# Kernel optimization log

Hardware: AMD Instinct MI355X
Metric: run time of the kernel (lower is better)

## Reference

```python
import jax, jax.numpy as jnp
import numpy as np

N, E, D_IN, H, D = 170000, 1200000, 128, 4, 32
NEG_SLOPE = 0.2


def setup_inputs() -> dict:
    key = jax.random.key(0)
    ks = jax.random.split(key, 8)
    x = jax.random.normal(ks[0], (N, D_IN), dtype=jnp.float32)
    # xavier-normal-ish scale for linear weights
    W_embed = jax.random.normal(ks[1], (D_IN, H * D), dtype=jnp.float32) * (2.0 / (D_IN + H * D)) ** 0.5
    a_src = jax.random.normal(ks[2], (H, D), dtype=jnp.float32) * (2.0 / (1 + H * D)) ** 0.5
    a_dst = jax.random.normal(ks[3], (H, D), dtype=jnp.float32) * (2.0 / (1 + H * D)) ** 0.5
    W_lin = jax.random.normal(ks[4], (D_IN, H * D), dtype=jnp.float32) * (2.0 / (D_IN + H * D)) ** 0.5
    bias = jnp.zeros((H * D,), dtype=jnp.float32)
    src = jax.random.randint(ks[5], (E,), 0, N, dtype=jnp.int32)
    dst = jax.random.randint(ks[6], (E,), 0, N, dtype=jnp.int32)
    return {"x": x, "W_embed": W_embed, "a_src": a_src, "a_dst": a_dst,
            "W_lin": W_lin, "bias": bias, "src": src, "dst": dst}


def reference(x, W_embed, a_src, a_dst, W_lin, bias, src, dst):
    n = x.shape[0]
    # node projections: [N, H, D]
    h = (x @ W_embed).reshape(n, H, D)
    dot_src = jnp.einsum('nhd,hd->nh', h, a_src)  # [N, H]
    dot_dst = jnp.einsum('nhd,hd->nh', h, a_dst)  # [N, H]
    # edge attention logits: leaky_relu(dot_src[u] + dot_dst[v])  [E, H]
    z = dot_src[src] + dot_dst[dst]
    logit = jnp.where(z >= 0, z, NEG_SLOPE * z)
    # edge softmax over incoming edges of each destination node
    m = jax.ops.segment_max(logit, dst, num_segments=n)          # [N, H]
    e = jnp.exp(logit - m[dst])                                   # [E, H]
    denom = jax.ops.segment_sum(e, dst, num_segments=n)          # [N, H]
    prob = e / denom[dst]                                         # [E, H]
    # weighted scatter-sum aggregation: sum_e prob_e * h[src_e]
    msg = h[src] * prob[:, :, None]                               # [E, H, D]
    out = jax.ops.segment_sum(msg, dst, num_segments=n)          # [N, H, D]
    out = out.reshape(n, H * D)
    out = out + x @ W_lin
    out = out + bias[None, :]
    return out
```

## Files before the change

### kernel.cpp

```cpp
#include <hip/hip_runtime.h>
#include <hip/hip_bf16.h>

static constexpr int   N_NODES   = 170000;
static constexpr int   E_EDGES   = 1200000;
static constexpr float NEG_SLOPE = 0.2f;

typedef __attribute__((ext_vector_type(8))) short bfrag8;
typedef __attribute__((ext_vector_type(4))) float facc4;

__device__ __forceinline__ short f2bf(float f) {
    __hip_bfloat16 h = __float2bfloat16(f);
    return *reinterpret_cast<short*>(&h);
}

__global__ void wt_init_kernel(const float* __restrict__ We,
                               const float* __restrict__ Wl,
                               const float* __restrict__ a_src,
                               const float* __restrict__ a_dst,
                               short* __restrict__ WtG,
                               int* __restrict__ deg)
{
    const int t = threadIdx.x;
    if (blockIdx.x < 128) {
        const int k = blockIdx.x;
        if (t < 128) WtG[t * 128 + k] = f2bf(We[k * 128 + t]);
        else         WtG[t * 128 + k] = f2bf(Wl[k * 128 + (t - 128)]);
    } else if (blockIdx.x < 136) {
        const int idx = (blockIdx.x - 128) * 256 + t;
        if (idx < 1024) {
            const int g = idx >> 7;
            const int k = idx & 127;
            const int hh = g & 3;
            const float* av = (g < 4) ? a_src : a_dst;
            float s = 0.f;
            #pragma unroll
            for (int d = 0; d < 32; ++d)
                s += We[k * 128 + hh * 32 + d] * av[hh * 32 + d];
            WtG[(256 + g) * 128 + k] = f2bf(s);
        } else {
            const int z = idx - 1024;
            WtG[(264 + (z >> 7)) * 128 + (z & 127)] = 0;
        }
    }
    const int i = blockIdx.x * 256 + t;
    if (i < N_NODES) deg[i] = 0;
}

__global__ void hist_kernel(const int* __restrict__ dst,
                            int* __restrict__ deg,
                            int* __restrict__ seq)
{
    int e = blockIdx.x * blockDim.x + threadIdx.x;
    if (e < E_EDGES) {
        const int s = atomicAdd(&deg[dst[e]], 1);
        __builtin_nontemporal_store(s, &seq[e]);
    }
}

__global__ __launch_bounds__(256) void scan_local_kernel(
    const int* __restrict__ deg, int* __restrict__ row_ptr, int* __restrict__ bsum)
{
    __shared__ int sh[256];
    const int t = threadIdx.x;
    const int base = blockIdx.x * 1024 + t * 4;
    int v0 = (base + 0 < N_NODES) ? deg[base + 0] : 0;
    int v1 = (base + 1 < N_NODES) ? deg[base + 1] : 0;
    int v2 = (base + 2 < N_NODES) ? deg[base + 2] : 0;
    int v3 = (base + 3 < N_NODES) ? deg[base + 3] : 0;
    const int tot = v0 + v1 + v2 + v3;
    sh[t] = tot;
    __syncthreads();
    for (int off = 1; off < 256; off <<= 1) {
        int add = (t >= off) ? sh[t - off] : 0;
        __syncthreads();
        sh[t] += add;
        __syncthreads();
    }
    const int excl = sh[t] - tot;
    if (base + 0 < N_NODES) row_ptr[base + 0] = excl;
    if (base + 1 < N_NODES) row_ptr[base + 1] = excl + v0;
    if (base + 2 < N_NODES) row_ptr[base + 2] = excl + v0 + v1;
    if (base + 3 < N_NODES) row_ptr[base + 3] = excl + v0 + v1 + v2;
    if (t == 255) bsum[blockIdx.x] = sh[255];
}

__global__ __launch_bounds__(256) void scan_block_kernel(
    const int* __restrict__ bsum, int* __restrict__ boff, int nblk)
{
    __shared__ int sh[256];
    const int t = threadIdx.x;
    const int v = (t < nblk) ? bsum[t] : 0;
    sh[t] = v;
    __syncthreads();
    for (int off = 1; off < 256; off <<= 1) {
        int add = (t >= off) ? sh[t - off] : 0;
        __syncthreads();
        sh[t] += add;
        __syncthreads();
    }
    boff[t] = sh[t] - v;
}

__global__ void scan_add_kernel(int* __restrict__ row_ptr,
                                const int* __restrict__ boff)
{
    int i = blockIdx.x * blockDim.x + threadIdx.x;
    if (i < N_NODES) row_ptr[i] += boff[i >> 10];
    if (i == 0) row_ptr[N_NODES] = E_EDGES;
}

__global__ void csr_place_kernel(const int* __restrict__ src,
                                 const int* __restrict__ dst,
                                 const int* __restrict__ seq,
                                 const int* __restrict__ rowp,
                                 int* __restrict__ srcs)
{
    int e = blockIdx.x * blockDim.x + threadIdx.x;
    if (e >= E_EDGES) return;
    const int p = rowp[dst[e]] + seq[e];
    __builtin_nontemporal_store(src[e], &srcs[p]);
}

static constexpr int LDB = 136;

__global__ __launch_bounds__(256, 4) void mfma_gemm_kernel(
    const float* __restrict__ x,
    const short* __restrict__ WtG,
    const float* __restrict__ bias,
    short* __restrict__ hbuf,
    float* __restrict__ dsrc,
    float* __restrict__ ddst,
    float* __restrict__ outp)
{
    __shared__ short Bs[144 * LDB];
    const int tid  = threadIdx.x;
    const long row0 = (long)blockIdx.x * 128;

    const int w    = tid >> 6;
    const int l    = tid & 63;
    const int col  = l & 15;
    const int quad = l >> 4;

    long ar0 = row0 + w * 32 + col;
    long ar1 = ar0 + 16;
    if (ar0 > N_NODES - 1) ar0 = N_NODES - 1;
    if (ar1 > N_NODES - 1) ar1 = N_NODES - 1;
    const float4* xp0 = (const float4*)&x[ar0 * 128 + quad * 8];
    const float4* xp1 = (const float4*)&x[ar1 * 128 + quad * 8];
    float4 av[2][4][2];
    #pragma unroll
    for (int ks = 0; ks < 4; ++ks) {
        av[0][ks][0] = xp0[ks * 8 + 0];
        av[0][ks][1] = xp0[ks * 8 + 1];
        av[1][ks][0] = xp1[ks * 8 + 0];
        av[1][ks][1] = xp1[ks * 8 + 1];
    }

    #pragma unroll
    for (int it = 0; it < 9; ++it) {
        const int idx = it * 256 + tid;
        const int n   = idx >> 4;
        const int kc  = (idx & 15) * 8;
        const int gn  = (n < 128) ? n : (n + 128);
        *(int4*)&Bs[n * LDB + kc] = *(const int4*)&WtG[gn * 128 + kc];
    }

    bfrag8 afr[2][4];
    #pragma unroll
    for (int m = 0; m < 2; ++m)
        #pragma unroll
        for (int ks = 0; ks < 4; ++ks) {
            bfrag8 t;
            t[0] = f2bf(av[m][ks][0].x); t[1] = f2bf(av[m][ks][0].y);
            t[2] = f2bf(av[m][ks][0].z); t[3] = f2bf(av[m][ks][0].w);
            t[4] = f2bf(av[m][ks][1].x); t[5] = f2bf(av[m][ks][1].y);
            t[6] = f2bf(av[m][ks][1].z); t[7] = f2bf(av[m][ks][1].w);
            afr[m][ks] = t;
        }
    __syncthreads();

    facc4 acc[2][8];
    facc4 adot[2];

    #pragma unroll
    for (int m = 0; m < 2; ++m) {
        adot[m] = (facc4)(0.f);
        #pragma unroll
        for (int t = 0; t < 8; ++t) acc[m][t] = (facc4)(0.f);
    }

    #pragma unroll
    for (int ks = 0; ks < 4; ++ks) {
        #pragma unroll
        for (int t = 0; t < 8; ++t) {
            const bfrag8 b = *(const bfrag8*)&Bs[(t * 16 + col) * LDB + ks * 32 + quad * 8];
            acc[0][t] = __builtin_amdgcn_mfma_f32_16x16x32_bf16(afr[0][ks], b, acc[0][t], 0, 0, 0);
            acc[1][t] = __builtin_amdgcn_mfma_f32_16x16x32_bf16(afr[1][ks], b, acc[1][t], 0, 0, 0);
        }
        const bfrag8 bd = *(const bfrag8*)&Bs[(128 + col) * LDB + ks * 32 + quad * 8];
        adot[0] = __builtin_amdgcn_mfma_f32_16x16x32_bf16(afr[0][ks], bd, adot[0], 0, 0, 0);
        adot[1] = __builtin_amdgcn_mfma_f32_16x16x32_bf16(afr[1][ks], bd, adot[1], 0, 0, 0);
    }

    #pragma unroll
    for (int m = 0; m < 2; ++m) {
        const long rbase = row0 + w * 32 + m * 16 + quad * 4;
        #pragma unroll
        for (int r = 0; r < 4; ++r) {
            const long mm = rbase + r;
            if (mm >= N_NODES) continue;
            #pragma unroll
            for (int t = 0; t < 8; ++t)
                hbuf[mm * 128 + t * 16 + col] = f2bf(acc[m][t][r]);
            if (col < 4)      dsrc[mm * 4 + col]       = adot[m][r];
            else if (col < 8) ddst[mm * 4 + (col - 4)] = adot[m][r];
        }
    }

    __syncthreads();
    #pragma unroll
    for (int it = 0; it < 8; ++it) {
        const int idx = it * 256 + tid;
        const int n   = idx >> 4;
        const int kc  = (idx & 15) * 8;
        *(int4*)&Bs[n * LDB + kc] = *(const int4*)&WtG[(128 + n) * 128 + kc];
    }
    __syncthreads();

    #pragma unroll
    for (int m = 0; m < 2; ++m)
        #pragma unroll
        for (int t = 0; t < 8; ++t) acc[m][t] = (facc4)(0.f);

    #pragma unroll
    for (int ks = 0; ks < 4; ++ks) {
        #pragma unroll
        for (int t = 0; t < 8; ++t) {
            const bfrag8 b = *(const bfrag8*)&Bs[(t * 16 + col) * LDB + ks * 32 + quad * 8];
            acc[0][t] = __builtin_amdgcn_mfma_f32_16x16x32_bf16(afr[0][ks], b, acc[0][t], 0, 0, 0);
            acc[1][t] = __builtin_amdgcn_mfma_f32_16x16x32_bf16(afr[1][ks], b, acc[1][t], 0, 0, 0);
        }
    }

    #pragma unroll
    for (int t = 0; t < 8; ++t) {
        const float bv = bias[t * 16 + col];
        #pragma unroll
        for (int m = 0; m < 2; ++m) {
            const long rbase = row0 + w * 32 + m * 16 + quad * 4;
            #pragma unroll
            for (int r = 0; r < 4; ++r) {
                const long mm = rbase + r;
                if (mm < N_NODES) outp[mm * 128 + t * 16 + col] = acc[m][t][r] + bv;
            }
        }
    }
}

__global__ __launch_bounds__(256) void agg_kernel(
    const int* __restrict__ row_ptr, const int* __restrict__ srcs,
    const float* __restrict__ dsrc, const float* __restrict__ ddst,
    const short* __restrict__ hbuf, float* __restrict__ outp)
{
    const long node = (long)blockIdx.x * 4 + (threadIdx.x >> 6);
    if (node >= N_NODES) return;
    const int lane   = threadIdx.x & 63;
    const int head_c = lane >> 4;
    const int c2     = lane << 1;
    const int slot   = lane >> 2;
    const int head_w = lane & 3;
    const int start = __builtin_amdgcn_readfirstlane(row_ptr[node]);
    const int end   = __builtin_amdgcn_readfirstlane(row_ptr[node + 1]);
    if (start == end) return;

    const float ddw = ddst[node * 4 + head_w];

    float a0 = 0.f, a1 = 0.f, dn = 0.f;

#define EDGE_BODY(i) \
    const float w##i = __shfl(wv, (k + i) * 4 + head_c); \
    const int   s##i = __builtin_amdgcn_readlane(sv, (k + i) * 4); \
    const uint  h##i = *(const uint*)&hbuf[(long)s##i * 128 + c2];

#define EDGE_ACC(i) { \
    dn += w##i; \
    a0 = fmaf(w##i, __uint_as_float(h##i << 16),         a0); \
    a1 = fmaf(w##i, __uint_as_float(h##i & 0xFFFF0000u), a1); }

    for (int j = start; j < end; j += 16) {
        const int idx = j + slot;
        const int ci  = (idx < end) ? idx : (end - 1);
        const int sv  = srcs[ci];
        float z = dsrc[sv * 4 + head_w] + ddw;
        z = fmaxf(z, NEG_SLOPE * z);
        float wv = __expf(z);
        if (idx >= end) wv = 0.f;
        const int chunk = (end - j < 16) ? (end - j) : 16;
        for (int k = 0; k < chunk; k += 4) {
            EDGE_BODY(0) EDGE_BODY(1) EDGE_BODY(2) EDGE_BODY(3)
            EDGE_ACC(0) EDGE_ACC(1) EDGE_ACC(2) EDGE_ACC(3)
        }
    }
#undef EDGE_BODY
#undef EDGE_ACC

    const float inv = 1.f / dn;
    float2* op = (float2*)&outp[node * 128 + c2];
    float2 o = *op;
    o.x += a0 * inv;
    o.y += a1 * inv;
    *op = o;
}

extern "C" void kernel_launch(void* const* d_in, const int* in_sizes, int n_in,
                              void* d_out, int out_size, void* d_ws, size_t ws_size,
                              hipStream_t stream)
{
    const float* x       = (const float*)d_in[0];
    const float* W_embed = (const float*)d_in[1];
    const float* a_src   = (const float*)d_in[2];
    const float* a_dst   = (const float*)d_in[3];
    const float* W_lin   = (const float*)d_in[4];
    const float* bias    = (const float*)d_in[5];
    const int*   src     = (const int*)d_in[6];
    const int*   dst     = (const int*)d_in[7];
    float* outp = (float*)d_out;

    char* ws = (char*)d_ws;
    short* WtG   = (short*)ws;  ws += (size_t)272 * 128 * sizeof(short);
    short* hbuf  = (short*)ws;  ws += (size_t)N_NODES * 128 * sizeof(short);
    int*   srcs  = (int*)ws;    ws += (size_t)E_EDGES * sizeof(int);
    float* dsrc  = (float*)ws;  ws += (size_t)N_NODES * 4 * sizeof(float);
    float* ddst  = (float*)ws;  ws += (size_t)N_NODES * 4 * sizeof(float);
    int*   deg   = (int*)ws;    ws += (size_t)N_NODES * sizeof(int);
    int*   rowp  = (int*)ws;    ws += (size_t)(N_NODES + 16) * sizeof(int);
    int*   bsum  = (int*)ws;    ws += 256 * sizeof(int);
    int*   boff  = (int*)ws;    ws += 256 * sizeof(int);

    int* seq = (int*)dsrc;

    const int SCAN_BLKS = (N_NODES + 1023) / 1024;

    wt_init_kernel<<<(N_NODES + 255) / 256, 256, 0, stream>>>(
        W_embed, W_lin, a_src, a_dst, WtG, deg);
    hist_kernel<<<(E_EDGES + 255) / 256, 256, 0, stream>>>(dst, deg, seq);
    scan_local_kernel<<<SCAN_BLKS, 256, 0, stream>>>(deg, rowp, bsum);
    scan_block_kernel<<<1, 256, 0, stream>>>(bsum, boff, SCAN_BLKS);
    scan_add_kernel<<<(N_NODES + 255) / 256, 256, 0, stream>>>(rowp, boff);

    csr_place_kernel<<<(E_EDGES + 255) / 256, 256, 0, stream>>>(
        src, dst, seq, rowp, srcs);

    mfma_gemm_kernel<<<(N_NODES + 127) / 128, 256, 0, stream>>>(
        x, WtG, bias, hbuf, dsrc, ddst, outp);

    agg_kernel<<<(N_NODES + 3) / 4, 256, 0, stream>>>(
        rowp, srcs, dsrc, ddst, hbuf, outp);
}
```

Measured before the change: 401.1 us.

## Merge block-scan into scan-add and split fused GEMM into embed/linear kernels

The single-block scan kernel is removed. Each scan_add block now computes its own offset by reducing the preceding block sums with wave shuffles, which saves one launch and one serialized tiny kernel. The fused GEMM, which computed both the embedding projection and the linear projection, is split into two kernels. The split lowers per-block LDS and register pressure and may improve occupancy, but x is now read twice from HBM.

```diff
diff --git a/kernel.cpp b/kernel.cpp
--- a/kernel.cpp
+++ b/kernel.cpp
@@ -84,29 +84,24 @@
     if (t == 255) bsum[blockIdx.x] = sh[255];
 }
 
-__global__ __launch_bounds__(256) void scan_block_kernel(
-    const int* __restrict__ bsum, int* __restrict__ boff, int nblk)
-{
-    __shared__ int sh[256];
-    const int t = threadIdx.x;
-    const int v = (t < nblk) ? bsum[t] : 0;
-    sh[t] = v;
+__global__ __launch_bounds__(256) void scan_add_kernel(
+    int* __restrict__ row_ptr, const int* __restrict__ bsum)
+{
+    const int t   = threadIdx.x;
+    const int blk = blockIdx.x;
+    int v = (t < blk) ? bsum[t] : 0;
+    #pragma unroll
+    for (int m = 32; m >= 1; m >>= 1) v += __shfl_xor(v, m, 64);
+    __shared__ int sh[4];
+    if ((t & 63) == 0) sh[t >> 6] = v;
     __syncthreads();
-    for (int off = 1; off < 256; off <<= 1) {
-        int add = (t >= off) ? sh[t - off] : 0;
-        __syncthreads();
-        sh[t] += add;
-        __syncthreads();
-    }
-    boff[t] = sh[t] - v;
-}
-
-__global__ void scan_add_kernel(int* __restrict__ row_ptr,
-                                const int* __restrict__ boff)
-{
-    int i = blockIdx.x * blockDim.x + threadIdx.x;
-    if (i < N_NODES) row_ptr[i] += boff[i >> 10];
-    if (i == 0) row_ptr[N_NODES] = E_EDGES;
+    const int boff = sh[0] + sh[1] + sh[2] + sh[3];
+
+    const int base = blk * 1024 + t * 4;
+    #pragma unroll
+    for (int q = 0; q < 4; ++q)
+        if (base + q < N_NODES) row_ptr[base + q] += boff;
+    if (blk == 0 && t == 0) row_ptr[N_NODES] = E_EDGES;
 }
 
 __global__ void csr_place_kernel(const int* __restrict__ src,
@@ -123,38 +118,52 @@
 
 static constexpr int LDB = 136;
 
-__global__ __launch_bounds__(256, 4) void mfma_gemm_kernel(
+#define LOAD_A_FRAGS                                                         \
+    long ar0 = row0 + w * 32 + col;                                          \
+    long ar1 = ar0 + 16;                                                     \
+    if (ar0 > N_NODES - 1) ar0 = N_NODES - 1;                                \
+    if (ar1 > N_NODES - 1) ar1 = N_NODES - 1;                                \
+    const float4* xp0 = (const float4*)&x[ar0 * 128 + quad * 8];             \
+    const float4* xp1 = (const float4*)&x[ar1 * 128 + quad * 8];             \
+    float4 av[2][4][2];                                                      \
+    _Pragma("unroll")                                                        \
+    for (int ks = 0; ks < 4; ++ks) {                                         \
+        av[0][ks][0] = xp0[ks * 8 + 0];                                      \
+        av[0][ks][1] = xp0[ks * 8 + 1];                                      \
+        av[1][ks][0] = xp1[ks * 8 + 0];                                      \
+        av[1][ks][1] = xp1[ks * 8 + 1];                                      \
+    }
+
+#define CONVERT_A_FRAGS                                                      \
+    bfrag8 afr[2][4];                                                        \
+    _Pragma("unroll")                                                        \
+    for (int m = 0; m < 2; ++m)                                              \
+        _Pragma("unroll")                                                    \
+        for (int ks = 0; ks < 4; ++ks) {                                     \
+            bfrag8 tv;                                                       \
+            tv[0] = f2bf(av[m][ks][0].x); tv[1] = f2bf(av[m][ks][0].y);      \
+            tv[2] = f2bf(av[m][ks][0].z); tv[3] = f2bf(av[m][ks][0].w);      \
+            tv[4] = f2bf(av[m][ks][1].x); tv[5] = f2bf(av[m][ks][1].y);      \
+            tv[6] = f2bf(av[m][ks][1].z); tv[7] = f2bf(av[m][ks][1].w);      \
+            afr[m][ks] = tv;                                                 \
+        }
+
+__global__ __launch_bounds__(256, 4) void embed_gemm_kernel(
     const float* __restrict__ x,
     const short* __restrict__ WtG,
-    const float* __restrict__ bias,
     short* __restrict__ hbuf,
     float* __restrict__ dsrc,
-    float* __restrict__ ddst,
-    float* __restrict__ outp)
+    float* __restrict__ ddst)
 {
     __shared__ short Bs[144 * LDB];
     const int tid  = threadIdx.x;
     const long row0 = (long)blockIdx.x * 128;
-
     const int w    = tid >> 6;
     const int l    = tid & 63;
     const int col  = l & 15;
     const int quad = l >> 4;
 
-    long ar0 = row0 + w * 32 + col;
-    long ar1 = ar0 + 16;
-    if (ar0 > N_NODES - 1) ar0 = N_NODES - 1;
-    if (ar1 > N_NODES - 1) ar1 = N_NODES - 1;
-    const float4* xp0 = (const float4*)&x[ar0 * 128 + quad * 8];
-    const float4* xp1 = (const float4*)&x[ar1 * 128 + quad * 8];
-    float4 av[2][4][2];
-    #pragma unroll
-    for (int ks = 0; ks < 4; ++ks) {
-        av[0][ks][0] = xp0[ks * 8 + 0];
-        av[0][ks][1] = xp0[ks * 8 + 1];
-        av[1][ks][0] = xp1[ks * 8 + 0];
-        av[1][ks][1] = xp1[ks * 8 + 1];
-    }
+    LOAD_A_FRAGS
 
     #pragma unroll
     for (int it = 0; it < 9; ++it) {
@@ -165,23 +174,11 @@
         *(int4*)&Bs[n * LDB + kc] = *(const int4*)&WtG[gn * 128 + kc];
     }
 
-    bfrag8 afr[2][4];
-    #pragma unroll
-    for (int m = 0; m < 2; ++m)
-        #pragma unroll
-        for (int ks = 0; ks < 4; ++ks) {
-            bfrag8 t;
-            t[0] = f2bf(av[m][ks][0].x); t[1] = f2bf(av[m][ks][0].y);
-            t[2] = f2bf(av[m][ks][0].z); t[3] = f2bf(av[m][ks][0].w);
-            t[4] = f2bf(av[m][ks][1].x); t[5] = f2bf(av[m][ks][1].y);
-            t[6] = f2bf(av[m][ks][1].z); t[7] = f2bf(av[m][ks][1].w);
-            afr[m][ks] = t;
-        }
+    CONVERT_A_FRAGS
     __syncthreads();
 
     facc4 acc[2][8];
     facc4 adot[2];
-
     #pragma unroll
     for (int m = 0; m < 2; ++m) {
         adot[m] = (facc4)(0.f);
@@ -216,8 +213,24 @@
             else if (col < 8) ddst[mm * 4 + (col - 4)] = adot[m][r];
         }
     }
-
-    __syncthreads();
+}
+
+__global__ __launch_bounds__(256, 4) void lin_gemm_kernel(
+    const float* __restrict__ x,
+    const short* __restrict__ WtG,
+    const float* __restrict__ bias,
+    float* __restrict__ outp)
+{
+    __shared__ short Bs[128 * LDB];
+    const int tid  = threadIdx.x;
+    const long row0 = (long)blockIdx.x * 128;
+    const int w    = tid >> 6;
+    const int l    = tid & 63;
+    const int col  = l & 15;
+    const int quad = l >> 4;
+
+    LOAD_A_FRAGS
+
     #pragma unroll
     for (int it = 0; it < 8; ++it) {
         const int idx = it * 256 + tid;
@@ -225,8 +238,11 @@
         const int kc  = (idx & 15) * 8;
         *(int4*)&Bs[n * LDB + kc] = *(const int4*)&WtG[(128 + n) * 128 + kc];
     }
+
+    CONVERT_A_FRAGS
     __syncthreads();
 
+    facc4 acc[2][8];
     #pragma unroll
     for (int m = 0; m < 2; ++m)
         #pragma unroll
@@ -335,7 +351,6 @@
     int*   deg   = (int*)ws;    ws += (size_t)N_NODES * sizeof(int);
     int*   rowp  = (int*)ws;    ws += (size_t)(N_NODES + 16) * sizeof(int);
     int*   bsum  = (int*)ws;    ws += 256 * sizeof(int);
-    int*   boff  = (int*)ws;    ws += 256 * sizeof(int);
 
     int* seq = (int*)dsrc;
 
@@ -345,14 +360,15 @@
         W_embed, W_lin, a_src, a_dst, WtG, deg);
     hist_kernel<<<(E_EDGES + 255) / 256, 256, 0, stream>>>(dst, deg, seq);
     scan_local_kernel<<<SCAN_BLKS, 256, 0, stream>>>(deg, rowp, bsum);
-    scan_block_kernel<<<1, 256, 0, stream>>>(bsum, boff, SCAN_BLKS);
-    scan_add_kernel<<<(N_NODES + 255) / 256, 256, 0, stream>>>(rowp, boff);
+    scan_add_kernel<<<SCAN_BLKS, 256, 0, stream>>>(rowp, bsum);
 
     csr_place_kernel<<<(E_EDGES + 255) / 256, 256, 0, stream>>>(
         src, dst, seq, rowp, srcs);
 
-    mfma_gemm_kernel<<<(N_NODES + 127) / 128, 256, 0, stream>>>(
-        x, WtG, bias, hbuf, dsrc, ddst, outp);
+    lin_gemm_kernel<<<(N_NODES + 127) / 128, 256, 0, stream>>>(
+        x, WtG, bias, outp);
+    embed_gemm_kernel<<<(N_NODES + 127) / 128, 256, 0, stream>>>(
+        x, WtG, hbuf, dsrc, ddst);
 
     agg_kernel<<<(N_NODES + 3) / 4, 256, 0, stream>>>(
         rowp, srcs, dsrc, ddst, hbuf, outp);
```

After: 402.8 us. About the same (+0.4%).
